# Kernel optimization log

Hardware: AMD Instinct MI355X
Metric: run time of the kernel (lower is better)

## Reference

```python
import jax, jax.numpy as jnp
import numpy as np

HIDDEN = 1024
BETA = 1.0
SPARSITY_THRESHOLD = 1.0


def _sparsemax(x):
    # Faithful port of the module's custom sparsemax (including its
    # nonstandard per-position tau). Operates over the last axis.
    n = x.shape[-1]
    z = x - jnp.max(x, axis=-1, keepdims=True)
    sum_z = jnp.sum(z, axis=-1, keepdims=True)
    step = (sum_z - 1.0) / n                       # step_size
    sorted_z = -jnp.sort(-z, axis=-1)              # descending sort
    cumsum_z = jnp.cumsum(sorted_z, axis=-1)
    is_gt = sorted_z > step
    rng = jnp.arange(1, n + 1, dtype=jnp.int32)
    k = jnp.max(rng * is_gt, axis=-1, keepdims=True).astype(x.dtype)
    tau = (cumsum_z - 1.0 - step * k) / k          # [.., n] per-position tau
    return jnp.clip(z - tau, 0.0)


def setup_inputs() -> dict:
    key = jax.random.key(0)
    kx, kq, kk, kv = jax.random.split(key, 4)
    B, S, D = 4, 2048, 1024
    x = jax.random.normal(kx, (B, S, D), dtype=jnp.float32)
    # torch Linear weight layout: [out_features, in_features]
    scale = 1.0 / np.sqrt(D)
    Wq = jax.random.normal(kq, (HIDDEN, D), dtype=jnp.float32) * scale
    Wk = jax.random.normal(kk, (HIDDEN, D), dtype=jnp.float32) * scale
    Wv = jax.random.normal(kv, (HIDDEN, D), dtype=jnp.float32) * scale
    return {"x": x, "Wq": Wq, "Wk": Wk, "Wv": Wv}


def reference(x, Wq, Wk, Wv):
    Q = jnp.einsum('bsd,hd->bsh', x, Wq)
    K = jnp.einsum('bsd,hd->bsh', x, Wk)
    V = jnp.einsum('bsd,hd->bsh', x, Wv)
    energy = jnp.einsum('bsh,bth->bst', Q, K) / jnp.sqrt(jnp.asarray(HIDDEN, x.dtype))
    scores = energy * BETA
    sparsity = jnp.mean(jnp.abs(x))
    attention = jax.lax.cond(
        sparsity < SPARSITY_THRESHOLD,
        _sparsemax,
        lambda s: jax.nn.softmax(s, axis=-1),
        scores,
    )
    return jnp.einsum('bst,bth->bsh', attention, V)
```

## Files before the change

### kernel.cpp

```cpp
#include <hip/hip_runtime.h>
#include <math.h>

#define B_   4
#define S_   2048
#define D_   1024
#define H_   1024
#define NROW 2048
#define TOTX 8388608.0f

typedef _Float16 f16x8 __attribute__((ext_vector_type(8)));
typedef float f32x4 __attribute__((ext_vector_type(4)));

__device__ __forceinline__ unsigned short f2h(float f) {
  _Float16 h = (_Float16)f;
  return __builtin_bit_cast(unsigned short, h);
}

#define GLD16(gp, lp)                                                            \
  __builtin_amdgcn_global_load_lds(                                              \
      (__attribute__((address_space(1))) void*)(gp),                             \
      (__attribute__((address_space(3))) void*)(lp), 16, 0, 0)

__global__ __launch_bounds__(256) void f2h_abs_kernel(const float* __restrict__ in,
                                                      unsigned short* __restrict__ out,
                                                      float* absOut, int n4) {
  int i0 = blockIdx.x * 256 + threadIdx.x;
  int stride = gridDim.x * 256;
  float s = 0.f;
  for (int i = i0; i < n4; i += stride) {
    float4 v = ((const float4*)in)[i];
    ushort4 o;
    o.x = f2h(v.x); o.y = f2h(v.y); o.z = f2h(v.z); o.w = f2h(v.w);
    ((ushort4*)out)[i] = o;
    s += fabsf(v.x) + fabsf(v.y) + fabsf(v.z) + fabsf(v.w);
  }
#pragma unroll
  for (int off = 32; off; off >>= 1) s += __shfl_xor(s, off);
  __shared__ float red[4];
  if ((threadIdx.x & 63) == 0) red[threadIdx.x >> 6] = s;
  __syncthreads();
  if (threadIdx.x == 0) atomicAdd(absOut, red[0] + red[1] + red[2] + red[3]);
}

__global__ __launch_bounds__(256) void f2h3_kernel(const float* __restrict__ a,
                                                   const float* __restrict__ b,
                                                   const float* __restrict__ c,
                                                   unsigned short* __restrict__ oa,
                                                   unsigned short* __restrict__ ob,
                                                   unsigned short* __restrict__ oc,
                                                   int n4) {
  int i = blockIdx.x * 256 + threadIdx.x;
  if (i >= n4) return;
  const float* in = (blockIdx.y == 0) ? a : (blockIdx.y == 1) ? b : c;
  unsigned short* out = (blockIdx.y == 0) ? oa : (blockIdx.y == 1) ? ob : oc;
  float4 v = ((const float4*)in)[i];
  ushort4 o;
  o.x = f2h(v.x); o.y = f2h(v.y); o.z = f2h(v.z); o.w = f2h(v.w);
  ((ushort4*)out)[i] = o;
}

__global__ __launch_bounds__(256) void transpose_h16(const unsigned short* __restrict__ in,
                                                     unsigned short* __restrict__ out,
                                                     int R, int C) {
  __shared__ unsigned short t[32][33];
  const int z = blockIdx.z;
  in  += (long long)z * R * C;
  out += (long long)z * R * C;
  const int c0 = blockIdx.x * 32, r0 = blockIdx.y * 32;
#pragma unroll
  for (int i = 0; i < 4; ++i) {
    int r = threadIdx.y + i * 8;
    t[r][threadIdx.x] = in[(long long)(r0 + r) * C + c0 + threadIdx.x];
  }
  __syncthreads();
#pragma unroll
  for (int i = 0; i < 4; ++i) {
    int r = threadIdx.y + i * 8;
    out[(long long)(c0 + r) * R + r0 + threadIdx.x] = t[threadIdx.x][r];
  }
}

template <int MI, bool OUT_F16>
__global__ __launch_bounds__(512, 2) void gemm8_nt(const unsigned short* __restrict__ A,
                                                   const unsigned short* __restrict__ B,
                                                   void* __restrict__ Cv,
                                                   int M, int N, int K,
                                                   long long sA, long long sB, long long sC,
                                                   float scale) {
  constexpr int BM  = MI * 32;
  constexpr int ASZ = BM * 32;
  constexpr int BSZ = 256 * 32;
  constexpr int TSZ = ASZ + BSZ;
  constexpr int MH  = MI / 2;

  const int bz = blockIdx.z;
  A += (long long)bz * sA;
  B += (long long)bz * sB;

  __shared__ __align__(16) unsigned short lds[2 * TSZ];

  const int tid = threadIdx.x;
  const int lane = tid & 63;
  const int w = tid >> 6;
  const int wr = w >> 2;
  const int wc = w & 3;
  const int m0 = blockIdx.y * BM, n0 = blockIdx.x * 256;

  f32x4 acc[MI][4] = {};

  const int srow = tid >> 2;
  const int scol = ((lane & 3) ^ ((lane >> 3) & 3)) * 8;
  const unsigned short* gA0 = A + (long long)(m0 + srow) * K + scol;
  const unsigned short* gA1 = gA0 + (long long)128 * K;
  const unsigned short* gB0 = B + (long long)(n0 + srow) * K + scol;
  const unsigned short* gB1 = gB0 + (long long)128 * K;
  const int wb = w * 512;

  const int fm = lane & 15;
  const int col8 = ((lane >> 4) ^ ((lane >> 1) & 3)) * 8;
  int aoff[MI], boff[4];
#pragma unroll
  for (int mi = 0; mi < MI; ++mi) aoff[mi] = (wr * (MI * 16) + mi * 16 + fm) * 32 + col8;
#pragma unroll
  for (int ni = 0; ni < 4; ++ni) boff[ni] = ASZ + (wc * 64 + ni * 16 + fm) * 32 + col8;

  const int nt = K >> 5;

#define STAGE(nb, k0)                                    \
  do {                                                   \
    unsigned short* L_ = lds + (nb) * TSZ;               \
    GLD16(gA0 + (k0), L_ + wb);                          \
    if (MI == 8) GLD16(gA1 + (k0), L_ + 4096 + wb);      \
    GLD16(gB0 + (k0), L_ + ASZ + wb);                    \
    GLD16(gB1 + (k0), L_ + ASZ + 4096 + wb);             \
  } while (0)

  STAGE(0, 0);
  STAGE(1, 32);
  if (MI == 8) asm volatile("s_waitcnt vmcnt(4)" ::: "memory");
  else         asm volatile("s_waitcnt vmcnt(3)" ::: "memory");
  __builtin_amdgcn_s_barrier();

  for (int t = 0; t < nt; ++t) {
    const unsigned short* L = lds + (t & 1) * TSZ;
    f16x8 af[MH], bf[4];
#pragma unroll
    for (int mi = 0; mi < MH; ++mi) af[mi] = *(const f16x8*)(L + aoff[mi]);
#pragma unroll
    for (int ni = 0; ni < 4; ++ni) bf[ni] = *(const f16x8*)(L + boff[ni]);
    __builtin_amdgcn_s_setprio(1);
#pragma unroll
    for (int mi = 0; mi < MH; ++mi)
#pragma unroll
      for (int ni = 0; ni < 4; ++ni)
        acc[mi][ni] = __builtin_amdgcn_mfma_f32_16x16x32_f16(af[mi], bf[ni],
                                                             acc[mi][ni], 0, 0, 0);
    __builtin_amdgcn_s_setprio(0);
    f16x8 ag[MH];
#pragma unroll
    for (int mi = 0; mi < MH; ++mi) ag[mi] = *(const f16x8*)(L + aoff[MH + mi]);
    asm volatile("s_waitcnt lgkmcnt(0)" ::: "memory");
    __builtin_amdgcn_sched_barrier(0);
    __builtin_amdgcn_s_barrier();
    if (t + 2 < nt) STAGE(t & 1, (t + 2) << 5);
    __builtin_amdgcn_s_setprio(1);
#pragma unroll
    for (int mi = 0; mi < MH; ++mi)
#pragma unroll
      for (int ni = 0; ni < 4; ++ni)
        acc[MH + mi][ni] = __builtin_amdgcn_mfma_f32_16x16x32_f16(ag[mi], bf[ni],
                                                                  acc[MH + mi][ni], 0, 0, 0);
    __builtin_amdgcn_s_setprio(0);
    if (t + 2 < nt) {
      if (MI == 8) asm volatile("s_waitcnt vmcnt(4)" ::: "memory");
      else         asm volatile("s_waitcnt vmcnt(3)" ::: "memory");
    } else if (t + 1 < nt) {
      asm volatile("s_waitcnt vmcnt(0)" ::: "memory");
    }
    __builtin_amdgcn_s_barrier();
  }
#undef STAGE

  const int cm = (lane >> 4) * 4;
  const int cn = lane & 15;
#pragma unroll
  for (int mi = 0; mi < MI; ++mi)
#pragma unroll
    for (int ni = 0; ni < 4; ++ni) {
#pragma unroll
      for (int r = 0; r < 4; ++r) {
        long long m = m0 + wr * (MI * 16) + mi * 16 + cm + r;
        long long n = n0 + wc * 64 + ni * 16 + cn;
        float v = acc[mi][ni][r] * scale;
        if (OUT_F16)
          ((unsigned short*)Cv)[(long long)bz * sC + m * N + n] = f2h(v);
        else
          ((float*)Cv)[(long long)bz * sC + m * N + n] = v;
      }
    }
}

template <int K, int J>
__device__ __forceinline__ void intra_s(float (&r)[32]) {
#pragma unroll
  for (int v = 0; v < 32; ++v)
    if ((v & J) == 0) {
      const int u = v | J;
      const bool dsc = ((v & K) == 0);
      float a = r[v], b = r[u];
      float mx = fmaxf(a, b), mn = fminf(a, b);
      r[v] = dsc ? mx : mn;
      r[u] = dsc ? mn : mx;
    }
}

template <int J>
__device__ __forceinline__ void intra_desc(float (&r)[32]) {
#pragma unroll
  for (int v = 0; v < 32; ++v)
    if ((v & J) == 0) {
      const int u = v | J;
      float a = r[v], b = r[u];
      r[v] = fmaxf(a, b);
      r[u] = fminf(a, b);
    }
}

template <int JL>
__device__ __forceinline__ void cross_desc(float (&r)[32], int lane, int bp32) {
  const bool keepmax = ((lane & JL) == 0);
  float b[32];
#pragma unroll
  for (int v = 0; v < 32; ++v) {
    int av = __builtin_bit_cast(int, r[v]);
    int bv;
    if constexpr (JL == 32)
      bv = __builtin_amdgcn_ds_bpermute(bp32, av);
    else
      bv = __builtin_amdgcn_ds_swizzle(av, (JL << 10) | 0x1F);
    b[v] = __builtin_bit_cast(float, bv);
  }
  __builtin_amdgcn_sched_barrier(0);
#pragma unroll
  for (int v = 0; v < 32; ++v) {
    float mx = fmaxf(r[v], b[v]), mn = fminf(r[v], b[v]);
    r[v] = keepmax ? mx : mn;
  }
}

__device__ __forceinline__ void signfix(float (&r)[32], unsigned fix) {
#pragma unroll
  for (int v = 0; v < 32; ++v)
    r[v] = __builtin_bit_cast(float, __builtin_bit_cast(unsigned, r[v]) ^ fix);
}

__global__ __launch_bounds__(256, 4) void attn_row_wave(const float* __restrict__ scores,
                                                        unsigned short* __restrict__ attn,
                                                        const float* __restrict__ absSum) {
  const int tid = threadIdx.x;
  const int lane = tid & 63;
  const int row = blockIdx.x * 4 + (tid >> 6);
  const float* rowp = scores + (long long)row * NROW;
  unsigned short* aout = attn + (long long)row * NROW;
  const int bp32 = (lane ^ 32) << 2;

  const float4* rp4 = (const float4*)rowp + lane * 8;
  float r[32];
  float lm = -INFINITY, lsraw = 0.f;
#pragma unroll
  for (int q = 0; q < 8; ++q) {
    float4 v = rp4[q];
    r[q * 4 + 0] = v.x; r[q * 4 + 1] = v.y;
    r[q * 4 + 2] = v.z; r[q * 4 + 3] = v.w;
    lm = fmaxf(lm, fmaxf(fmaxf(v.x, v.y), fmaxf(v.z, v.w)));
    lsraw += v.x + v.y + v.z + v.w;
  }
#pragma unroll
  for (int off = 32; off; off >>= 1) {
    lm = fmaxf(lm, __shfl_xor(lm, off, 64));
    lsraw += __shfl_xor(lsraw, off, 64);
  }

  const bool use_softmax = (absSum[0] * (1.0f / TOTX)) >= 1.0f;

  if (use_softmax) {
    float ls = 0.f;
#pragma unroll
    for (int v = 0; v < 32; ++v) { r[v] = expf(r[v] - lm); ls += r[v]; }
#pragma unroll
    for (int off = 32; off; off >>= 1) ls += __shfl_xor(ls, off, 64);
    float inv = 1.0f / ls;
    ushort4* op = (ushort4*)(aout + lane * 32);
#pragma unroll
    for (int q = 0; q < 8; ++q) {
      ushort4 o;
      o.x = f2h(r[q * 4 + 0] * inv); o.y = f2h(r[q * 4 + 1] * inv);
      o.z = f2h(r[q * 4 + 2] * inv); o.w = f2h(r[q * 4 + 3] * inv);
      op[q] = o;
    }
    return;
  }

#pragma unroll
  for (int v = 0; v < 32; ++v) r[v] -= lm;
  const float step = ((lsraw - (float)NROW * lm) - 1.0f) * (1.0f / (float)NROW);

  intra_s<2, 1>(r);
  intra_s<4, 2>(r); intra_s<4, 1>(r);
  intra_s<8, 4>(r); intra_s<8, 2>(r); intra_s<8, 1>(r);
  intra_s<16, 8>(r); intra_s<16, 4>(r); intra_s<16, 2>(r); intra_s<16, 1>(r);

  unsigned cur = (unsigned)(lane & 1) << 31;
  signfix(r, cur);
  intra_desc<16>(r); intra_desc<8>(r); intra_desc<4>(r);
  intra_desc<2>(r); intra_desc<1>(r);

  { unsigned want = (unsigned)(lane & 2) << 30;
    signfix(r, cur ^ want); cur = want; }
  cross_desc<1>(r, lane, bp32);
  intra_desc<16>(r); intra_desc<8>(r); intra_desc<4>(r);
  intra_desc<2>(r); intra_desc<1>(r);

  { unsigned want = (unsigned)(lane & 4) << 29;
    signfix(r, cur ^ want); cur = want; }
  cross_desc<2>(r, lane, bp32); cross_desc<1>(r, lane, bp32);
  intra_desc<16>(r); intra_desc<8>(r); intra_desc<4>(r);
  intra_desc<2>(r); intra_desc<1>(r);

  { unsigned want = (unsigned)(lane & 8) << 28;
    signfix(r, cur ^ want); cur = want; }
  cross_desc<4>(r, lane, bp32); cross_desc<2>(r, lane, bp32);
  cross_desc<1>(r, lane, bp32);
  intra_desc<16>(r); intra_desc<8>(r); intra_desc<4>(r);
  intra_desc<2>(r); intra_desc<1>(r);

  { unsigned want = (unsigned)(lane & 16) << 27;
    signfix(r, cur ^ want); cur = want; }
  cross_desc<8>(r, lane, bp32); cross_desc<4>(r, lane, bp32);
  cross_desc<2>(r, lane, bp32); cross_desc<1>(r, lane, bp32);
  intra_desc<16>(r); intra_desc<8>(r); intra_desc<4>(r);
  intra_desc<2>(r); intra_desc<1>(r);

  { unsigned want = (unsigned)(lane & 32) << 26;
    signfix(r, cur ^ want); cur = want; }
  cross_desc<16>(r, lane, bp32); cross_desc<8>(r, lane, bp32);
  cross_desc<4>(r, lane, bp32); cross_desc<2>(r, lane, bp32);
  cross_desc<1>(r, lane, bp32);
  intra_desc<16>(r); intra_desc<8>(r); intra_desc<4>(r);
  intra_desc<2>(r); intra_desc<1>(r);

  signfix(r, cur);
  cross_desc<32>(r, lane, bp32); cross_desc<16>(r, lane, bp32);
  cross_desc<8>(r, lane, bp32); cross_desc<4>(r, lane, bp32);
  cross_desc<2>(r, lane, bp32); cross_desc<1>(r, lane, bp32);
  intra_desc<16>(r); intra_desc<8>(r); intra_desc<4>(r);
  intra_desc<2>(r); intra_desc<1>(r);

  float lcnt = 0.f;
#pragma unroll
  for (int v = 0; v < 32; ++v) lcnt += (r[v] > step) ? 1.0f : 0.0f;
#pragma unroll
  for (int off = 32; off; off >>= 1) lcnt += __shfl_xor(lcnt, off, 64);
  const float kf = lcnt;

  float run = 0.f;
#pragma unroll
  for (int v = 0; v < 32; ++v) { run += r[v]; r[v] = run; }
  float pre = run;
#pragma unroll
  for (int off = 1; off < 64; off <<= 1) {
    float t = __shfl_up(pre, off, 64);
    if (lane >= off) pre += t;
  }
  pre -= run;
#pragma unroll
  for (int v = 0; v < 32; ++v) r[v] += pre;

  const float inv_k = 1.0f / kf;
  const float c1 = 1.0f + step * kf;

  unsigned long long up = (unsigned long long)rowp;
  asm volatile("" : "+v"(up));
  const float4* rp4e = (const float4*)up + lane * 8;
  ushort4* op = (ushort4*)(aout + lane * 32);
#pragma unroll
  for (int q = 0; q < 8; ++q) {
    float4 v = rp4e[q];
    ushort4 o;
    o.x = f2h(fmaxf((v.x - lm) - (r[q * 4 + 0] - c1) * inv_k, 0.0f));
    o.y = f2h(fmaxf((v.y - lm) - (r[q * 4 + 1] - c1) * inv_k, 0.0f));
    o.z = f2h(fmaxf((v.z - lm) - (r[q * 4 + 2] - c1) * inv_k, 0.0f));
    o.w = f2h(fmaxf((v.w - lm) - (r[q * 4 + 3] - c1) * inv_k, 0.0f));
    op[q] = o;
  }
}

extern "C" void kernel_launch(void* const* d_in, const int* in_sizes, int n_in,
                              void* d_out, int out_size, void* d_ws, size_t ws_size,
                              hipStream_t stream) {
  const float* x  = (const float*)d_in[0];
  const float* Wq = (const float*)d_in[1];
  const float* Wk = (const float*)d_in[2];
  const float* Wv = (const float*)d_in[3];
  float* out = (float*)d_out;

  const long long NX = (long long)B_ * S_ * D_;
  const long long NW = (long long)H_ * D_;

  char* base = (char*)d_ws;
  unsigned short* x16  = (unsigned short*)(base);
  unsigned short* Wq16 = (unsigned short*)(base + (16ll << 20));
  unsigned short* Wk16 = (unsigned short*)(base + (18ll << 20));
  unsigned short* Wv16 = (unsigned short*)(base + (20ll << 20));
  float*          Sc   = (float*)(base);
  unsigned short* Vt16 = (unsigned short*)(base + (64ll << 20));
  unsigned short* Q16  = (unsigned short*)(base + (80ll << 20));
  unsigned short* K16  = (unsigned short*)(base + (96ll << 20));
  unsigned short* V16  = (unsigned short*)(base + (112ll << 20));
  unsigned short* A16  = (unsigned short*)(base + (80ll << 20));
  float*          flag = (float*)(base + (144ll << 20));

  hipMemsetAsync(flag, 0, sizeof(float), stream);

  f2h_abs_kernel<<<1024, 256, 0, stream>>>(x, x16, flag, (int)(NX / 4));
  f2h3_kernel<<<dim3((int)(NW / 4 + 255) / 256, 3), 256, 0, stream>>>(
      Wq, Wk, Wv, Wq16, Wk16, Wv16, (int)(NW / 4));

  {
    dim3 grid(H_ / 256, (B_ * S_) / 128, 3);
    gemm8_nt<4, true><<<grid, 512, 0, stream>>>(x16, Wq16, Q16, B_ * S_, H_, D_,
                                                0, (long long)NW, (long long)(8ll << 20),
                                                1.0f);
  }

  {
    dim3 grid(H_ / 32, S_ / 32, B_);
    transpose_h16<<<grid, dim3(32, 8), 0, stream>>>(V16, Vt16, S_, H_);
  }

  {
    dim3 grid(S_ / 256, S_ / 256, B_);
    gemm8_nt<8, false><<<grid, 512, 0, stream>>>(Q16, K16, Sc, S_, S_, H_,
                                                 (long long)S_ * H_, (long long)S_ * H_,
                                                 (long long)S_ * S_, 1.0f / 32.0f);
  }

  attn_row_wave<<<(B_ * S_) / 4, 256, 0, stream>>>(Sc, A16, flag);

  {
    dim3 grid(H_ / 256, S_ / 128, B_);
    gemm8_nt<4, false><<<grid, 512, 0, stream>>>(A16, Vt16, out, S_, H_, S_,
                                                 (long long)S_ * S_, (long long)H_ * S_,
                                                 (long long)S_ * H_, 1.0f);
  }
}
```

Baseline: 338.0 us.

## Triple-buffer GEMM LDS pipeline and process two rows per wave in sparsemax

```diff
diff --git a/kernel.cpp b/kernel.cpp
--- a/kernel.cpp
+++ b/kernel.cpp
@@ -81,12 +81,13 @@
 }
 
 template <int MI, bool OUT_F16>
-__global__ __launch_bounds__(512, 2) void gemm8_nt(const unsigned short* __restrict__ A,
-                                                   const unsigned short* __restrict__ B,
-                                                   void* __restrict__ Cv,
-                                                   int M, int N, int K,
-                                                   long long sA, long long sB, long long sC,
-                                                   float scale) {
+__global__ __launch_bounds__(512, MI == 4 ? 4 : 2)
+void gemm8_nt(const unsigned short* __restrict__ A,
+              const unsigned short* __restrict__ B,
+              void* __restrict__ Cv,
+              int M, int N, int K,
+              long long sA, long long sB, long long sC,
+              float scale) {
   constexpr int BM  = MI * 32;
   constexpr int ASZ = BM * 32;
   constexpr int BSZ = 256 * 32;
@@ -97,7 +98,7 @@
   A += (long long)bz * sA;
   B += (long long)bz * sB;
 
-  __shared__ __align__(16) unsigned short lds[2 * TSZ];
+  __shared__ __align__(16) unsigned short lds[3 * TSZ];
 
   const int tid = threadIdx.x;
   const int lane = tid & 63;
@@ -126,28 +127,47 @@
 
   const int nt = K >> 5;
 
-#define STAGE(nb, k0)                                    \
-  do {                                                   \
-    unsigned short* L_ = lds + (nb) * TSZ;               \
-    GLD16(gA0 + (k0), L_ + wb);                          \
-    if (MI == 8) GLD16(gA1 + (k0), L_ + 4096 + wb);      \
-    GLD16(gB0 + (k0), L_ + ASZ + wb);                    \
-    GLD16(gB1 + (k0), L_ + ASZ + 4096 + wb);             \
+#define STAGE_ALL(nb, k0)                                      \
+  do {                                                         \
+    unsigned short* L_ = lds + (nb) * TSZ;                     \
+    if (MI == 8) {                                             \
+      GLD16(gA0 + (k0), L_ + wb);                              \
+      GLD16(gA1 + (k0), L_ + 4096 + wb);                       \
+      GLD16(gB0 + (k0), L_ + ASZ + wb);                        \
+      GLD16(gB1 + (k0), L_ + ASZ + 4096 + wb);                 \
+    } else {                                                   \
+      GLD16(gA0 + (k0), L_ + wb);                              \
+      GLD16(gB0 + (k0), L_ + ASZ + wb);                        \
+      GLD16(gB1 + (k0), L_ + ASZ + 4096 + wb);                 \
+    }                                                          \
   } while (0)
 
-  STAGE(0, 0);
-  STAGE(1, 32);
+  STAGE_ALL(0, 0);
+  STAGE_ALL(1, 32);
   if (MI == 8) asm volatile("s_waitcnt vmcnt(4)" ::: "memory");
   else         asm volatile("s_waitcnt vmcnt(3)" ::: "memory");
   __builtin_amdgcn_s_barrier();
 
+  int b0 = 0, b1 = 1, b2 = 2;
   for (int t = 0; t < nt; ++t) {
-    const unsigned short* L = lds + (t & 1) * TSZ;
+    const unsigned short* L = lds + b0 * TSZ;
+    unsigned short* Ls = lds + b2 * TSZ;
+    const bool st = (t + 2 < nt);
+    const int k2 = (t + 2) << 5;
+
     f16x8 af[MH], bf[4];
 #pragma unroll
     for (int mi = 0; mi < MH; ++mi) af[mi] = *(const f16x8*)(L + aoff[mi]);
 #pragma unroll
     for (int ni = 0; ni < 4; ++ni) bf[ni] = *(const f16x8*)(L + boff[ni]);
+    if (st) {
+      if (MI == 8) { GLD16(gA0 + k2, Ls + wb); GLD16(gA1 + k2, Ls + 4096 + wb); }
+      else         { GLD16(gA0 + k2, Ls + wb); GLD16(gB0 + k2, Ls + ASZ + wb); }
+    }
+    __builtin_amdgcn_sched_barrier(0);
+    __builtin_amdgcn_s_barrier();
+    asm volatile("s_waitcnt lgkmcnt(0)" ::: "memory");
+    __builtin_amdgcn_sched_barrier(0);
     __builtin_amdgcn_s_setprio(1);
 #pragma unroll
     for (int mi = 0; mi < MH; ++mi)
@@ -156,13 +176,25 @@
         acc[mi][ni] = __builtin_amdgcn_mfma_f32_16x16x32_f16(af[mi], bf[ni],
                                                              acc[mi][ni], 0, 0, 0);
     __builtin_amdgcn_s_setprio(0);
+    __builtin_amdgcn_s_barrier();
+
     f16x8 ag[MH];
 #pragma unroll
     for (int mi = 0; mi < MH; ++mi) ag[mi] = *(const f16x8*)(L + aoff[MH + mi]);
+    if (st) {
+      if (MI == 8) { GLD16(gB0 + k2, Ls + ASZ + wb); GLD16(gB1 + k2, Ls + ASZ + 4096 + wb); }
+      else         { GLD16(gB1 + k2, Ls + ASZ + 4096 + wb); }
+    }
+    if (st) {
+      if (MI == 8) asm volatile("s_waitcnt vmcnt(4)" ::: "memory");
+      else         asm volatile("s_waitcnt vmcnt(3)" ::: "memory");
+    } else if (t + 1 < nt) {
+      asm volatile("s_waitcnt vmcnt(0)" ::: "memory");
+    }
+    __builtin_amdgcn_sched_barrier(0);
+    __builtin_amdgcn_s_barrier();
     asm volatile("s_waitcnt lgkmcnt(0)" ::: "memory");
     __builtin_amdgcn_sched_barrier(0);
-    __builtin_amdgcn_s_barrier();
-    if (t + 2 < nt) STAGE(t & 1, (t + 2) << 5);
     __builtin_amdgcn_s_setprio(1);
 #pragma unroll
     for (int mi = 0; mi < MH; ++mi)
@@ -171,15 +203,11 @@
         acc[MH + mi][ni] = __builtin_amdgcn_mfma_f32_16x16x32_f16(ag[mi], bf[ni],
                                                                   acc[MH + mi][ni], 0, 0, 0);
     __builtin_amdgcn_s_setprio(0);
-    if (t + 2 < nt) {
-      if (MI == 8) asm volatile("s_waitcnt vmcnt(4)" ::: "memory");
-      else         asm volatile("s_waitcnt vmcnt(3)" ::: "memory");
-    } else if (t + 1 < nt) {
-      asm volatile("s_waitcnt vmcnt(0)" ::: "memory");
-    }
     __builtin_amdgcn_s_barrier();
-  }
-#undef STAGE
+
+    int tb = b0; b0 = b1; b1 = b2; b2 = tb;
+  }
+#undef STAGE_ALL
 
   const int cm = (lane >> 4) * 4;
   const int cn = lane & 15;
@@ -201,197 +229,234 @@
 }
 
 template <int K, int J>
-__device__ __forceinline__ void intra_s(float (&r)[32]) {
-#pragma unroll
-  for (int v = 0; v < 32; ++v)
-    if ((v & J) == 0) {
-      const int u = v | J;
-      const bool dsc = ((v & K) == 0);
-      float a = r[v], b = r[u];
-      float mx = fmaxf(a, b), mn = fminf(a, b);
-      r[v] = dsc ? mx : mn;
-      r[u] = dsc ? mn : mx;
-    }
+__device__ __forceinline__ void intra_s2(float (&r)[2][32]) {
+#pragma unroll
+  for (int h = 0; h < 2; ++h)
+#pragma unroll
+    for (int v = 0; v < 32; ++v)
+      if ((v & J) == 0) {
+        const int u = v | J;
+        const bool dsc = ((v & K) == 0);
+        float a = r[h][v], b = r[h][u];
+        float mx = fmaxf(a, b), mn = fminf(a, b);
+        r[h][v] = dsc ? mx : mn;
+        r[h][u] = dsc ? mn : mx;
+      }
 }
 
 template <int J>
-__device__ __forceinline__ void intra_desc(float (&r)[32]) {
-#pragma unroll
-  for (int v = 0; v < 32; ++v)
-    if ((v & J) == 0) {
-      const int u = v | J;
-      float a = r[v], b = r[u];
-      r[v] = fmaxf(a, b);
-      r[u] = fminf(a, b);
-    }
+__device__ __forceinline__ void intra_desc2(float (&r)[2][32]) {
+#pragma unroll
+  for (int h = 0; h < 2; ++h)
+#pragma unroll
+    for (int v = 0; v < 32; ++v)
+      if ((v & J) == 0) {
+        const int u = v | J;
+        float a = r[h][v], b = r[h][u];
+        r[h][v] = fmaxf(a, b);
+        r[h][u] = fminf(a, b);
+      }
 }
 
 template <int JL>
-__device__ __forceinline__ void cross_desc(float (&r)[32], int lane, int bp32) {
+__device__ __forceinline__ void cross_desc2(float (&r)[2][32], int lane, int bp32) {
   const bool keepmax = ((lane & JL) == 0);
-  float b[32];
-#pragma unroll
-  for (int v = 0; v < 32; ++v) {
-    int av = __builtin_bit_cast(int, r[v]);
-    int bv;
-    if constexpr (JL == 32)
-      bv = __builtin_amdgcn_ds_bpermute(bp32, av);
-    else
-      bv = __builtin_amdgcn_ds_swizzle(av, (JL << 10) | 0x1F);
-    b[v] = __builtin_bit_cast(float, bv);
-  }
+  float b[2][32];
+#pragma unroll
+  for (int h = 0; h < 2; ++h)
+#pragma unroll
+    for (int v = 0; v < 32; ++v) {
+      int av = __builtin_bit_cast(int, r[h][v]);
+      int bv;
+      if constexpr (JL == 32)
+        bv = __builtin_amdgcn_ds_bpermute(bp32, av);
+      else
+        bv = __builtin_amdgcn_ds_swizzle(av, (JL << 10) | 0x1F);
+      b[h][v] = __builtin_bit_cast(float, bv);
+    }
   __builtin_amdgcn_sched_barrier(0);
 #pragma unroll
-  for (int v = 0; v < 32; ++v) {
-    float mx = fmaxf(r[v], b[v]), mn = fminf(r[v], b[v]);
-    r[v] = keepmax ? mx : mn;
-  }
-}
-
-__device__ __forceinline__ void signfix(float (&r)[32], unsigned fix) {
-#pragma unroll
-  for (int v = 0; v < 32; ++v)
-    r[v] = __builtin_bit_cast(float, __builtin_bit_cast(unsigned, r[v]) ^ fix);
-}
-
-__global__ __launch_bounds__(256, 4) void attn_row_wave(const float* __restrict__ scores,
+  for (int h = 0; h < 2; ++h)
+#pragma unroll
+    for (int v = 0; v < 32; ++v) {
+      float mx = fmaxf(r[h][v], b[h][v]), mn = fminf(r[h][v], b[h][v]);
+      r[h][v] = keepmax ? mx : mn;
+    }
+}
+
+__device__ __forceinline__ void signfix2(float (&r)[2][32], unsigned fix) {
+#pragma unroll
+  for (int h = 0; h < 2; ++h)
+#pragma unroll
+    for (int v = 0; v < 32; ++v)
+      r[h][v] = __builtin_bit_cast(float, __builtin_bit_cast(unsigned, r[h][v]) ^ fix);
+}
+
+__global__ __launch_bounds__(256, 3) void attn_row_wave(const float* __restrict__ scores,
                                                         unsigned short* __restrict__ attn,
                                                         const float* __restrict__ absSum) {
   const int tid = threadIdx.x;
   const int lane = tid & 63;
-  const int row = blockIdx.x * 4 + (tid >> 6);
-  const float* rowp = scores + (long long)row * NROW;
-  unsigned short* aout = attn + (long long)row * NROW;
+  const int rbase = blockIdx.x * 8 + (tid >> 6) * 2;
+  const float* rowp = scores + (long long)rbase * NROW;
+  unsigned short* aout = attn + (long long)rbase * NROW;
   const int bp32 = (lane ^ 32) << 2;
 
-  const float4* rp4 = (const float4*)rowp + lane * 8;
-  float r[32];
-  float lm = -INFINITY, lsraw = 0.f;
-#pragma unroll
-  for (int q = 0; q < 8; ++q) {
-    float4 v = rp4[q];
-    r[q * 4 + 0] = v.x; r[q * 4 + 1] = v.y;
-    r[q * 4 + 2] = v.z; r[q * 4 + 3] = v.w;
-    lm = fmaxf(lm, fmaxf(fmaxf(v.x, v.y), fmaxf(v.z, v.w)));
-    lsraw += v.x + v.y + v.z + v.w;
+  float r[2][32];
+  float lm[2] = {-INFINITY, -INFINITY};
+  float ls[2] = {0.f, 0.f};
+#pragma unroll
+  for (int h = 0; h < 2; ++h) {
+    const float4* rp4 = (const float4*)(rowp + h * NROW) + lane * 8;
+#pragma unroll
+    for (int q = 0; q < 8; ++q) {
+      float4 v = rp4[q];
+      r[h][q * 4 + 0] = v.x; r[h][q * 4 + 1] = v.y;
+      r[h][q * 4 + 2] = v.z; r[h][q * 4 + 3] = v.w;
+      lm[h] = fmaxf(lm[h], fmaxf(fmaxf(v.x, v.y), fmaxf(v.z, v.w)));
+      ls[h] += v.x + v.y + v.z + v.w;
+    }
   }
 #pragma unroll
   for (int off = 32; off; off >>= 1) {
-    lm = fmaxf(lm, __shfl_xor(lm, off, 64));
-    lsraw += __shfl_xor(lsraw, off, 64);
+#pragma unroll
+    for (int h = 0; h < 2; ++h) {
+      lm[h] = fmaxf(lm[h], __shfl_xor(lm[h], off, 64));
+      ls[h] += __shfl_xor(ls[h], off, 64);
+    }
   }
 
   const bool use_softmax = (absSum[0] * (1.0f / TOTX)) >= 1.0f;
 
   if (use_softmax) {
-    float ls = 0.f;
-#pragma unroll
-    for (int v = 0; v < 32; ++v) { r[v] = expf(r[v] - lm); ls += r[v]; }
-#pragma unroll
-    for (int off = 32; off; off >>= 1) ls += __shfl_xor(ls, off, 64);
-    float inv = 1.0f / ls;
-    ushort4* op = (ushort4*)(aout + lane * 32);
-#pragma unroll
-    for (int q = 0; q < 8; ++q) {
-      ushort4 o;
-      o.x = f2h(r[q * 4 + 0] * inv); o.y = f2h(r[q * 4 + 1] * inv);
-      o.z = f2h(r[q * 4 + 2] * inv); o.w = f2h(r[q * 4 + 3] * inv);
-      op[q] = o;
+    float sum[2] = {0.f, 0.f};
+#pragma unroll
+    for (int h = 0; h < 2; ++h)
+#pragma unroll
+      for (int v = 0; v < 32; ++v) { r[h][v] = expf(r[h][v] - lm[h]); sum[h] += r[h][v]; }
+#pragma unroll
+    for (int off = 32; off; off >>= 1)
+#pragma unroll
+      for (int h = 0; h < 2; ++h) sum[h] += __shfl_xor(sum[h], off, 64);
+#pragma unroll
+    for (int h = 0; h < 2; ++h) {
+      float inv = 1.0f / sum[h];
+      ushort4* op = (ushort4*)(aout + h * NROW + lane * 32);
+#pragma unroll
+      for (int q = 0; q < 8; ++q) {
+        ushort4 o;
+        o.x = f2h(r[h][q * 4 + 0] * inv); o.y = f2h(r[h][q * 4 + 1] * inv);
+        o.z = f2h(r[h][q * 4 + 2] * inv); o.w = f2h(r[h][q * 4 + 3] * inv);
+        op[q] = o;
+      }
     }
     return;
   }
 
-#pragma unroll
-  for (int v = 0; v < 32; ++v) r[v] -= lm;
-  const float step = ((lsraw - (float)NROW * lm) - 1.0f) * (1.0f / (float)NROW);
-
-  intra_s<2, 1>(r);
-  intra_s<4, 2>(r); intra_s<4, 1>(r);
-  intra_s<8, 4>(r); intra_s<8, 2>(r); intra_s<8, 1>(r);
-  intra_s<16, 8>(r); intra_s<16, 4>(r); intra_s<16, 2>(r); intra_s<16, 1>(r);
+  float step[2];
+#pragma unroll
+  for (int h = 0; h < 2; ++h) {
+#pragma unroll
+    for (int v = 0; v < 32; ++v) r[h][v] -= lm[h];
+    step[h] = ((ls[h] - (float)NROW * lm[h]) - 1.0f) * (1.0f / (float)NROW);
+  }
+
+  intra_s2<2, 1>(r);
+  intra_s2<4, 2>(r); intra_s2<4, 1>(r);
+  intra_s2<8, 4>(r); intra_s2<8, 2>(r); intra_s2<8, 1>(r);
+  intra_s2<16, 8>(r); intra_s2<16, 4>(r); intra_s2<16, 2>(r); intra_s2<16, 1>(r);
 
   unsigned cur = (unsigned)(lane & 1) << 31;
-  signfix(r, cur);
-  intra_desc<16>(r); intra_desc<8>(r); intra_desc<4>(r);
-  intra_desc<2>(r); intra_desc<1>(r);
+  signfix2(r, cur);
+  intra_desc2<16>(r); intra_desc2<8>(r); intra_desc2<4>(r);
+  intra_desc2<2>(r); intra_desc2<1>(r);
 
   { unsigned want = (unsigned)(lane & 2) << 30;
-    signfix(r, cur ^ want); cur = want; }
-  cross_desc<1>(r, lane, bp32);
-  intra_desc<16>(r); intra_desc<8>(r); intra_desc<4>(r);
-  intra_desc<2>(r); intra_desc<1>(r);
+    signfix2(r, cur ^ want); cur = want; }
+  cross_desc2<1>(r, lane, bp32);
+  intra_desc2<16>(r); intra_desc2<8>(r); intra_desc2<4>(r);
+  intra_desc2<2>(r); intra_desc2<1>(r);
 
   { unsigned want = (unsigned)(lane & 4) << 29;
-    signfix(r, cur ^ want); cur = want; }
-  cross_desc<2>(r, lane, bp32); cross_desc<1>(r, lane, bp32);
-  intra_desc<16>(r); intra_desc<8>(r); intra_desc<4>(r);
-  intra_desc<2>(r); intra_desc<1>(r);
+    signfix2(r, cur ^ want); cur = want; }
+  cross_desc2<2>(r, lane, bp32); cross_desc2<1>(r, lane, bp32);
+  intra_desc2<16>(r); intra_desc2<8>(r); intra_desc2<4>(r);
+  intra_desc2<2>(r); intra_desc2<1>(r);
 
   { unsigned want = (unsigned)(lane & 8) << 28;
-    signfix(r, cur ^ want); cur = want; }
-  cross_desc<4>(r, lane, bp32); cross_desc<2>(r, lane, bp32);
-  cross_desc<1>(r, lane, bp32);
-  intra_desc<16>(r); intra_desc<8>(r); intra_desc<4>(r);
-  intra_desc<2>(r); intra_desc<1>(r);
+    signfix2(r, cur ^ want); cur = want; }
+  cross_desc2<4>(r, lane, bp32); cross_desc2<2>(r, lane, bp32);
+  cross_desc2<1>(r, lane, bp32);
+  intra_desc2<16>(r); intra_desc2<8>(r); intra_desc2<4>(r);
+  intra_desc2<2>(r); intra_desc2<1>(r);
 
   { unsigned want = (unsigned)(lane & 16) << 27;
-    signfix(r, cur ^ want); cur = want; }
-  cross_desc<8>(r, lane, bp32); cross_desc<4>(r, lane, bp32);
-  cross_desc<2>(r, lane, bp32); cross_desc<1>(r, lane, bp32);
-  intra_desc<16>(r); intra_desc<8>(r); intra_desc<4>(r);
-  intra_desc<2>(r); intra_desc<1>(r);
+    signfix2(r, cur ^ want); cur = want; }
+  cross_desc2<8>(r, lane, bp32); cross_desc2<4>(r, lane, bp32);
+  cross_desc2<2>(r, lane, bp32); cross_desc2<1>(r, lane, bp32);
+  intra_desc2<16>(r); intra_desc2<8>(r); intra_desc2<4>(r);
+  intra_desc2<2>(r); intra_desc2<1>(r);
 
   { unsigned want = (unsigned)(lane & 32) << 26;
-    signfix(r, cur ^ want); cur = want; }
-  cross_desc<16>(r, lane, bp32); cross_desc<8>(r, lane, bp32);
-  cross_desc<4>(r, lane, bp32); cross_desc<2>(r, lane, bp32);
-  cross_desc<1>(r, lane, bp32);
-  intra_desc<16>(r); intra_desc<8>(r); intra_desc<4>(r);
-  intra_desc<2>(r); intra_desc<1>(r);
-
-  signfix(r, cur);
-  cross_desc<32>(r, lane, bp32); cross_desc<16>(r, lane, bp32);
-  cross_desc<8>(r, lane, bp32); cross_desc<4>(r, lane, bp32);
-  cross_desc<2>(r, lane, bp32); cross_desc<1>(r, lane, bp32);
-  intra_desc<16>(r); intra_desc<8>(r); intra_desc<4>(r);
-  intra_desc<2>(r); intra_desc<1>(r);
-
-  float lcnt = 0.f;
-#pragma unroll
-  for (int v = 0; v < 32; ++v) lcnt += (r[v] > step) ? 1.0f : 0.0f;
-#pragma unroll
-  for (int off = 32; off; off >>= 1) lcnt += __shfl_xor(lcnt, off, 64);
-  const float kf = lcnt;
-
-  float run = 0.f;
-#pragma unroll
-  for (int v = 0; v < 32; ++v) { run += r[v]; r[v] = run; }
-  float pre = run;
-#pragma unroll
-  for (int off = 1; off < 64; off <<= 1) {
-    float t = __shfl_up(pre, off, 64);
-    if (lane >= off) pre += t;
-  }
-  pre -= run;
-#pragma unroll
-  for (int v = 0; v < 32; ++v) r[v] += pre;
-
-  const float inv_k = 1.0f / kf;
-  const float c1 = 1.0f + step * kf;
+    signfix2(r, cur ^ want); cur = want; }
+  cross_desc2<16>(r, lane, bp32); cross_desc2<8>(r, lane, bp32);
+  cross_desc2<4>(r, lane, bp32); cross_desc2<2>(r, lane, bp32);
+  cross_desc2<1>(r, lane, bp32);
+  intra_desc2<16>(r); intra_desc2<8>(r); intra_desc2<4>(r);
+  intra_desc2<2>(r); intra_desc2<1>(r);
+
+  signfix2(r, cur);
+  cross_desc2<32>(r, lane, bp32); cross_desc2<16>(r, lane, bp32);
+  cross_desc2<8>(r, lane, bp32); cross_desc2<4>(r, lane, bp32);
+  cross_desc2<2>(r, lane, bp32); cross_desc2<1>(r, lane, bp32);
+  intra_desc2<16>(r); intra_desc2<8>(r); intra_desc2<4>(r);
+  intra_desc2<2>(r); intra_desc2<1>(r);
+
+  float kf[2];
+#pragma unroll
+  for (int h = 0; h < 2; ++h) {
+    float lcnt = 0.f;
+#pragma unroll
+    for (int v = 0; v < 32; ++v) lcnt += (r[h][v] > step[h]) ? 1.0f : 0.0f;
+#pragma unroll
+    for (int off = 32; off; off >>= 1) lcnt += __shfl_xor(lcnt, off, 64);
+    kf[h] = lcnt;
+  }
+
+#pragma unroll
+  for (int h = 0; h < 2; ++h) {
+    float run = 0.f;
+#pragma unroll
+    for (int v = 0; v < 32; ++v) { run += r[h][v]; r[h][v] = run; }
+    float pre = run;
+#pragma unroll
+    for (int off = 1; off < 64; off <<= 1) {
+      float t = __shfl_up(pre, off, 64);
+      if (lane >= off) pre += t;
+    }
+    pre -= run;
+#pragma unroll
+    for (int v = 0; v < 32; ++v) r[h][v] += pre;
+  }
 
   unsigned long long up = (unsigned long long)rowp;
   asm volatile("" : "+v"(up));
-  const float4* rp4e = (const float4*)up + lane * 8;
-  ushort4* op = (ushort4*)(aout + lane * 32);
-#pragma unroll
-  for (int q = 0; q < 8; ++q) {
-    float4 v = rp4e[q];
-    ushort4 o;
-    o.x = f2h(fmaxf((v.x - lm) - (r[q * 4 + 0] - c1) * inv_k, 0.0f));
-    o.y = f2h(fmaxf((v.y - lm) - (r[q * 4 + 1] - c1) * inv_k, 0.0f));
-    o.z = f2h(fmaxf((v.z - lm) - (r[q * 4 + 2] - c1) * inv_k, 0.0f));
-    o.w = f2h(fmaxf((v.w - lm) - (r[q * 4 + 3] - c1) * inv_k, 0.0f));
-    op[q] = o;
+#pragma unroll
+  for (int h = 0; h < 2; ++h) {
+    const float inv_k = 1.0f / kf[h];
+    const float c1 = 1.0f + step[h] * kf[h];
+    const float4* rp4e = (const float4*)(up + (unsigned long long)h * NROW * 4) + lane * 8;
+    ushort4* op = (ushort4*)(aout + h * NROW + lane * 32);
+#pragma unroll
+    for (int q = 0; q < 8; ++q) {
+      float4 v = rp4e[q];
+      ushort4 o;
+      o.x = f2h(fmaxf((v.x - lm[h]) - (r[h][q * 4 + 0] - c1) * inv_k, 0.0f));
+      o.y = f2h(fmaxf((v.y - lm[h]) - (r[h][q * 4 + 1] - c1) * inv_k, 0.0f));
+      o.z = f2h(fmaxf((v.z - lm[h]) - (r[h][q * 4 + 2] - c1) * inv_k, 0.0f));
+      o.w = f2h(fmaxf((v.w - lm[h]) - (r[h][q * 4 + 3] - c1) * inv_k, 0.0f));
+      op[q] = o;
+    }
   }
 }
 
@@ -445,7 +510,7 @@
                                                  (long long)S_ * S_, 1.0f / 32.0f);
   }
 
-  attn_row_wave<<<(B_ * S_) / 4, 256, 0, stream>>>(Sc, A16, flag);
+  attn_row_wave<<<(B_ * S_) / 8, 256, 0, stream>>>(Sc, A16, flag);
 
   {
     dim3 grid(H_ / 256, S_ / 128, B_);
```

New measurement: 365.3 us. 1.08x slower.

## Sort each sparsemax row with a full workgroup instead of one wave

Applied to the files above, without the earlier changes.

```diff
diff --git a/kernel.cpp b/kernel.cpp
--- a/kernel.cpp
+++ b/kernel.cpp
@@ -10,6 +10,7 @@
 
 typedef _Float16 f16x8 __attribute__((ext_vector_type(8)));
 typedef float f32x4 __attribute__((ext_vector_type(4)));
+typedef unsigned short us8 __attribute__((ext_vector_type(8)));
 
 __device__ __forceinline__ unsigned short f2h(float f) {
   _Float16 h = (_Float16)f;
@@ -201,9 +202,9 @@
 }
 
 template <int K, int J>
-__device__ __forceinline__ void intra_s(float (&r)[32]) {
-#pragma unroll
-  for (int v = 0; v < 32; ++v)
+__device__ __forceinline__ void p_intra_s(float (&r)[8]) {
+#pragma unroll
+  for (int v = 0; v < 8; ++v)
     if ((v & J) == 0) {
       const int u = v | J;
       const bool dsc = ((v & K) == 0);
@@ -215,9 +216,9 @@
 }
 
 template <int J>
-__device__ __forceinline__ void intra_desc(float (&r)[32]) {
-#pragma unroll
-  for (int v = 0; v < 32; ++v)
+__device__ __forceinline__ void p_intra_d(float (&r)[8]) {
+#pragma unroll
+  for (int v = 0; v < 8; ++v)
     if ((v & J) == 0) {
       const int u = v | J;
       float a = r[v], b = r[u];
@@ -226,173 +227,187 @@
     }
 }
 
-template <int JL>
-__device__ __forceinline__ void cross_desc(float (&r)[32], int lane, int bp32) {
-  const bool keepmax = ((lane & JL) == 0);
-  float b[32];
-#pragma unroll
-  for (int v = 0; v < 32; ++v) {
+template <int LJ>
+__device__ __forceinline__ void p_cross_d(float (&r)[8], int lane, int bp32) {
+  const bool keepmax = ((lane & LJ) == 0);
+  float b[8];
+#pragma unroll
+  for (int v = 0; v < 8; ++v) {
     int av = __builtin_bit_cast(int, r[v]);
     int bv;
-    if constexpr (JL == 32)
+    if constexpr (LJ == 32)
       bv = __builtin_amdgcn_ds_bpermute(bp32, av);
     else
-      bv = __builtin_amdgcn_ds_swizzle(av, (JL << 10) | 0x1F);
+      bv = __builtin_amdgcn_ds_swizzle(av, (LJ << 10) | 0x1F);
     b[v] = __builtin_bit_cast(float, bv);
   }
   __builtin_amdgcn_sched_barrier(0);
 #pragma unroll
-  for (int v = 0; v < 32; ++v) {
+  for (int v = 0; v < 8; ++v) {
     float mx = fmaxf(r[v], b[v]), mn = fminf(r[v], b[v]);
     r[v] = keepmax ? mx : mn;
   }
 }
 
-__device__ __forceinline__ void signfix(float (&r)[32], unsigned fix) {
-#pragma unroll
-  for (int v = 0; v < 32; ++v)
+__device__ __forceinline__ void p_lds_d(float (&r)[8], float* LB, int tid, int wv, int WJ) {
+  const bool keepmax = ((wv & WJ) == 0);
+  __syncthreads();
+  float4* my = (float4*)(LB + tid * 8);
+  my[0] = make_float4(r[0], r[1], r[2], r[3]);
+  my[1] = make_float4(r[4], r[5], r[6], r[7]);
+  __syncthreads();
+  const float4* pp = (const float4*)(LB + (tid ^ (WJ << 6)) * 8);
+  float4 p0 = pp[0], p1 = pp[1];
+  float p[8] = {p0.x, p0.y, p0.z, p0.w, p1.x, p1.y, p1.z, p1.w};
+#pragma unroll
+  for (int v = 0; v < 8; ++v) {
+    float mx = fmaxf(r[v], p[v]), mn = fminf(r[v], p[v]);
+    r[v] = keepmax ? mx : mn;
+  }
+}
+
+__device__ __forceinline__ void sf8(float (&r)[8], unsigned fix) {
+#pragma unroll
+  for (int v = 0; v < 8; ++v)
     r[v] = __builtin_bit_cast(float, __builtin_bit_cast(unsigned, r[v]) ^ fix);
 }
 
-__global__ __launch_bounds__(256, 4) void attn_row_wave(const float* __restrict__ scores,
+__global__ __launch_bounds__(256, 6) void attn_row_wave(const float* __restrict__ scores,
                                                         unsigned short* __restrict__ attn,
                                                         const float* __restrict__ absSum) {
+  __shared__ float LB[2048];
+  __shared__ float red[8];
   const int tid = threadIdx.x;
   const int lane = tid & 63;
-  const int row = blockIdx.x * 4 + (tid >> 6);
+  const int wv = tid >> 6;
+  const int row = blockIdx.x;
   const float* rowp = scores + (long long)row * NROW;
   unsigned short* aout = attn + (long long)row * NROW;
   const int bp32 = (lane ^ 32) << 2;
 
-  const float4* rp4 = (const float4*)rowp + lane * 8;
-  float r[32];
-  float lm = -INFINITY, lsraw = 0.f;
-#pragma unroll
-  for (int q = 0; q < 8; ++q) {
-    float4 v = rp4[q];
-    r[q * 4 + 0] = v.x; r[q * 4 + 1] = v.y;
-    r[q * 4 + 2] = v.z; r[q * 4 + 3] = v.w;
-    lm = fmaxf(lm, fmaxf(fmaxf(v.x, v.y), fmaxf(v.z, v.w)));
-    lsraw += v.x + v.y + v.z + v.w;
-  }
+  const float4* rp4 = (const float4*)rowp + tid * 2;
+  float4 v0 = rp4[0], v1 = rp4[1];
+  float r[8] = {v0.x, v0.y, v0.z, v0.w, v1.x, v1.y, v1.z, v1.w};
+
+  float lm = fmaxf(fmaxf(fmaxf(r[0], r[1]), fmaxf(r[2], r[3])),
+                   fmaxf(fmaxf(r[4], r[5]), fmaxf(r[6], r[7])));
+  float ls = r[0] + r[1] + r[2] + r[3] + r[4] + r[5] + r[6] + r[7];
 #pragma unroll
   for (int off = 32; off; off >>= 1) {
     lm = fmaxf(lm, __shfl_xor(lm, off, 64));
-    lsraw += __shfl_xor(lsraw, off, 64);
-  }
+    ls += __shfl_xor(ls, off, 64);
+  }
+  if (lane == 0) { red[wv] = lm; red[4 + wv] = ls; }
+  __syncthreads();
+  lm = fmaxf(fmaxf(red[0], red[1]), fmaxf(red[2], red[3]));
+  ls = red[4] + red[5] + red[6] + red[7];
 
   const bool use_softmax = (absSum[0] * (1.0f / TOTX)) >= 1.0f;
 
   if (use_softmax) {
-    float ls = 0.f;
-#pragma unroll
-    for (int v = 0; v < 32; ++v) { r[v] = expf(r[v] - lm); ls += r[v]; }
-#pragma unroll
-    for (int off = 32; off; off >>= 1) ls += __shfl_xor(ls, off, 64);
-    float inv = 1.0f / ls;
-    ushort4* op = (ushort4*)(aout + lane * 32);
-#pragma unroll
-    for (int q = 0; q < 8; ++q) {
-      ushort4 o;
-      o.x = f2h(r[q * 4 + 0] * inv); o.y = f2h(r[q * 4 + 1] * inv);
-      o.z = f2h(r[q * 4 + 2] * inv); o.w = f2h(r[q * 4 + 3] * inv);
-      op[q] = o;
-    }
+    float s = 0.f;
+#pragma unroll
+    for (int v = 0; v < 8; ++v) { r[v] = expf(r[v] - lm); s += r[v]; }
+#pragma unroll
+    for (int off = 32; off; off >>= 1) s += __shfl_xor(s, off, 64);
+    __syncthreads();
+    if (lane == 0) red[wv] = s;
+    __syncthreads();
+    float inv = 1.0f / (red[0] + red[1] + red[2] + red[3]);
+    us8 o;
+#pragma unroll
+    for (int v = 0; v < 8; ++v) o[v] = f2h(r[v] * inv);
+    *(us8*)(aout + tid * 8) = o;
     return;
   }
 
 #pragma unroll
-  for (int v = 0; v < 32; ++v) r[v] -= lm;
-  const float step = ((lsraw - (float)NROW * lm) - 1.0f) * (1.0f / (float)NROW);
-
-  intra_s<2, 1>(r);
-  intra_s<4, 2>(r); intra_s<4, 1>(r);
-  intra_s<8, 4>(r); intra_s<8, 2>(r); intra_s<8, 1>(r);
-  intra_s<16, 8>(r); intra_s<16, 4>(r); intra_s<16, 2>(r); intra_s<16, 1>(r);
-
-  unsigned cur = (unsigned)(lane & 1) << 31;
-  signfix(r, cur);
-  intra_desc<16>(r); intra_desc<8>(r); intra_desc<4>(r);
-  intra_desc<2>(r); intra_desc<1>(r);
-
-  { unsigned want = (unsigned)(lane & 2) << 30;
-    signfix(r, cur ^ want); cur = want; }
-  cross_desc<1>(r, lane, bp32);
-  intra_desc<16>(r); intra_desc<8>(r); intra_desc<4>(r);
-  intra_desc<2>(r); intra_desc<1>(r);
-
-  { unsigned want = (unsigned)(lane & 4) << 29;
-    signfix(r, cur ^ want); cur = want; }
-  cross_desc<2>(r, lane, bp32); cross_desc<1>(r, lane, bp32);
-  intra_desc<16>(r); intra_desc<8>(r); intra_desc<4>(r);
-  intra_desc<2>(r); intra_desc<1>(r);
-
-  { unsigned want = (unsigned)(lane & 8) << 28;
-    signfix(r, cur ^ want); cur = want; }
-  cross_desc<4>(r, lane, bp32); cross_desc<2>(r, lane, bp32);
-  cross_desc<1>(r, lane, bp32);
-  intra_desc<16>(r); intra_desc<8>(r); intra_desc<4>(r);
-  intra_desc<2>(r); intra_desc<1>(r);
-
-  { unsigned want = (unsigned)(lane & 16) << 27;
-    signfix(r, cur ^ want); cur = want; }
-  cross_desc<8>(r, lane, bp32); cross_desc<4>(r, lane, bp32);
-  cross_desc<2>(r, lane, bp32); cross_desc<1>(r, lane, bp32);
-  intra_desc<16>(r); intra_desc<8>(r); intra_desc<4>(r);
-  intra_desc<2>(r); intra_desc<1>(r);
-
-  { unsigned want = (unsigned)(lane & 32) << 26;
-    signfix(r, cur ^ want); cur = want; }
-  cross_desc<16>(r, lane, bp32); cross_desc<8>(r, lane, bp32);
-  cross_desc<4>(r, lane, bp32); cross_desc<2>(r, lane, bp32);
-  cross_desc<1>(r, lane, bp32);
-  intra_desc<16>(r); intra_desc<8>(r); intra_desc<4>(r);
-  intra_desc<2>(r); intra_desc<1>(r);
-
-  signfix(r, cur);
-  cross_desc<32>(r, lane, bp32); cross_desc<16>(r, lane, bp32);
-  cross_desc<8>(r, lane, bp32); cross_desc<4>(r, lane, bp32);
-  cross_desc<2>(r, lane, bp32); cross_desc<1>(r, lane, bp32);
-  intra_desc<16>(r); intra_desc<8>(r); intra_desc<4>(r);
-  intra_desc<2>(r); intra_desc<1>(r);
+  for (int v = 0; v < 8; ++v) r[v] -= lm;
+  const float step = ((ls - (float)NROW * lm) - 1.0f) * (1.0f / (float)NROW);
+
+  p_intra_s<2, 1>(r);
+  p_intra_s<4, 2>(r); p_intra_s<4, 1>(r);
+
+  unsigned cur;
+  cur = (tid & 1) ? 0x80000000u : 0u; sf8(r, cur);
+  p_intra_d<4>(r); p_intra_d<2>(r); p_intra_d<1>(r);
+  { unsigned want = (tid & 2) ? 0x80000000u : 0u; sf8(r, cur ^ want); cur = want; }
+  p_cross_d<1>(r, lane, bp32);
+  p_intra_d<4>(r); p_intra_d<2>(r); p_intra_d<1>(r);
+  { unsigned want = (tid & 4) ? 0x80000000u : 0u; sf8(r, cur ^ want); cur = want; }
+  p_cross_d<2>(r, lane, bp32); p_cross_d<1>(r, lane, bp32);
+  p_intra_d<4>(r); p_intra_d<2>(r); p_intra_d<1>(r);
+  { unsigned want = (tid & 8) ? 0x80000000u : 0u; sf8(r, cur ^ want); cur = want; }
+  p_cross_d<4>(r, lane, bp32); p_cross_d<2>(r, lane, bp32); p_cross_d<1>(r, lane, bp32);
+  p_intra_d<4>(r); p_intra_d<2>(r); p_intra_d<1>(r);
+  { unsigned want = (tid & 16) ? 0x80000000u : 0u; sf8(r, cur ^ want); cur = want; }
+  p_cross_d<8>(r, lane, bp32); p_cross_d<4>(r, lane, bp32);
+  p_cross_d<2>(r, lane, bp32); p_cross_d<1>(r, lane, bp32);
+  p_intra_d<4>(r); p_intra_d<2>(r); p_intra_d<1>(r);
+  { unsigned want = (tid & 32) ? 0x80000000u : 0u; sf8(r, cur ^ want); cur = want; }
+  p_cross_d<16>(r, lane, bp32); p_cross_d<8>(r, lane, bp32); p_cross_d<4>(r, lane, bp32);
+  p_cross_d<2>(r, lane, bp32); p_cross_d<1>(r, lane, bp32);
+  p_intra_d<4>(r); p_intra_d<2>(r); p_intra_d<1>(r);
+  { unsigned want = (tid & 64) ? 0x80000000u : 0u; sf8(r, cur ^ want); cur = want; }
+  p_cross_d<32>(r, lane, bp32); p_cross_d<16>(r, lane, bp32); p_cross_d<8>(r, lane, bp32);
+  p_cross_d<4>(r, lane, bp32); p_cross_d<2>(r, lane, bp32); p_cross_d<1>(r, lane, bp32);
+  p_intra_d<4>(r); p_intra_d<2>(r); p_intra_d<1>(r);
+  { unsigned want = (tid & 128) ? 0x80000000u : 0u; sf8(r, cur ^ want); cur = want; }
+  p_lds_d(r, LB, tid, wv, 1);
+  p_cross_d<32>(r, lane, bp32); p_cross_d<16>(r, lane, bp32); p_cross_d<8>(r, lane, bp32);
+  p_cross_d<4>(r, lane, bp32); p_cross_d<2>(r, lane, bp32); p_cross_d<1>(r, lane, bp32);
+  p_intra_d<4>(r); p_intra_d<2>(r); p_intra_d<1>(r);
+  sf8(r, cur); cur = 0;
+  p_lds_d(r, LB, tid, wv, 2);
+  p_lds_d(r, LB, tid, wv, 1);
+  p_cross_d<32>(r, lane, bp32); p_cross_d<16>(r, lane, bp32); p_cross_d<8>(r, lane, bp32);
+  p_cross_d<4>(r, lane, bp32); p_cross_d<2>(r, lane, bp32); p_cross_d<1>(r, lane, bp32);
+  p_intra_d<4>(r); p_intra_d<2>(r); p_intra_d<1>(r);
 
   float lcnt = 0.f;
 #pragma unroll
-  for (int v = 0; v < 32; ++v) lcnt += (r[v] > step) ? 1.0f : 0.0f;
+  for (int v = 0; v < 8; ++v) lcnt += (r[v] > step) ? 1.0f : 0.0f;
 #pragma unroll
   for (int off = 32; off; off >>= 1) lcnt += __shfl_xor(lcnt, off, 64);
-  const float kf = lcnt;
 
   float run = 0.f;
 #pragma unroll
-  for (int v = 0; v < 32; ++v) { run += r[v]; r[v] = run; }
-  float pre = run;
+  for (int v = 0; v < 8; ++v) { run += r[v]; r[v] = run; }
+  float sc = run;
 #pragma unroll
   for (int off = 1; off < 64; off <<= 1) {
-    float t = __shfl_up(pre, off, 64);
-    if (lane >= off) pre += t;
-  }
-  pre -= run;
-#pragma unroll
-  for (int v = 0; v < 32; ++v) r[v] += pre;
-
-  const float inv_k = 1.0f / kf;
-  const float c1 = 1.0f + step * kf;
+    float t = __shfl_up(sc, off, 64);
+    if (lane >= off) sc += t;
+  }
+  const float tex = sc - run;
+
+  __syncthreads();
+  if (lane == 0)  red[wv] = lcnt;
+  if (lane == 63) red[4 + wv] = sc;
+  __syncthreads();
+  const float kf = red[0];
+  const float kfull = red[0] + red[1] + red[2] + red[3];
+  (void)kf;
+  float wex = 0.f;
+  if (wv > 0) wex += red[4];
+  if (wv > 1) wex += red[5];
+  if (wv > 2) wex += red[6];
+#pragma unroll
+  for (int v = 0; v < 8; ++v) r[v] += tex + wex;
+
+  const float inv_k = 1.0f / kfull;
+  const float c1 = 1.0f + step * kfull;
 
   unsigned long long up = (unsigned long long)rowp;
   asm volatile("" : "+v"(up));
-  const float4* rp4e = (const float4*)up + lane * 8;
-  ushort4* op = (ushort4*)(aout + lane * 32);
-#pragma unroll
-  for (int q = 0; q < 8; ++q) {
-    float4 v = rp4e[q];
-    ushort4 o;
-    o.x = f2h(fmaxf((v.x - lm) - (r[q * 4 + 0] - c1) * inv_k, 0.0f));
-    o.y = f2h(fmaxf((v.y - lm) - (r[q * 4 + 1] - c1) * inv_k, 0.0f));
-    o.z = f2h(fmaxf((v.z - lm) - (r[q * 4 + 2] - c1) * inv_k, 0.0f));
-    o.w = f2h(fmaxf((v.w - lm) - (r[q * 4 + 3] - c1) * inv_k, 0.0f));
-    op[q] = o;
-  }
+  const float4* rp4e = (const float4*)up + tid * 2;
+  float4 w0 = rp4e[0], w1 = rp4e[1];
+  float zo[8] = {w0.x, w0.y, w0.z, w0.w, w1.x, w1.y, w1.z, w1.w};
+  us8 o;
+#pragma unroll
+  for (int v = 0; v < 8; ++v)
+    o[v] = f2h(fmaxf((zo[v] - lm) - (r[v] - c1) * inv_k, 0.0f));
+  *(us8*)(aout + tid * 8) = o;
 }
 
 extern "C" void kernel_launch(void* const* d_in, const int* in_sizes, int n_in,
@@ -445,7 +460,7 @@
                                                  (long long)S_ * S_, 1.0f / 32.0f);
   }
 
-  attn_row_wave<<<(B_ * S_) / 4, 256, 0, stream>>>(Sc, A16, flag);
+  attn_row_wave<<<B_ * S_, 256, 0, stream>>>(Sc, A16, flag);
 
   {
     dim3 grid(H_ / 256, S_ / 128, B_);
```

Measured after the change: 354.2 us. +4.8%, slower.

## Fuse V transpose into projection GEMM epilogue and shrink QK^T tile

Applied to the files above, without the earlier changes.

```diff
diff --git a/kernel.cpp b/kernel.cpp
--- a/kernel.cpp
+++ b/kernel.cpp
@@ -59,31 +59,11 @@
   ((ushort4*)out)[i] = o;
 }
 
-__global__ __launch_bounds__(256) void transpose_h16(const unsigned short* __restrict__ in,
-                                                     unsigned short* __restrict__ out,
-                                                     int R, int C) {
-  __shared__ unsigned short t[32][33];
-  const int z = blockIdx.z;
-  in  += (long long)z * R * C;
-  out += (long long)z * R * C;
-  const int c0 = blockIdx.x * 32, r0 = blockIdx.y * 32;
-#pragma unroll
-  for (int i = 0; i < 4; ++i) {
-    int r = threadIdx.y + i * 8;
-    t[r][threadIdx.x] = in[(long long)(r0 + r) * C + c0 + threadIdx.x];
-  }
-  __syncthreads();
-#pragma unroll
-  for (int i = 0; i < 4; ++i) {
-    int r = threadIdx.y + i * 8;
-    out[(long long)(c0 + r) * R + r0 + threadIdx.x] = t[threadIdx.x][r];
-  }
-}
-
 template <int MI, bool OUT_F16>
 __global__ __launch_bounds__(512, 2) void gemm8_nt(const unsigned short* __restrict__ A,
                                                    const unsigned short* __restrict__ B,
                                                    void* __restrict__ Cv,
+                                                   unsigned short* __restrict__ VT,
                                                    int M, int N, int K,
                                                    long long sA, long long sB, long long sC,
                                                    float scale) {
@@ -183,6 +163,23 @@
 
   const int cm = (lane >> 4) * 4;
   const int cn = lane & 15;
+  if (VT != nullptr && bz == 2) {
+#pragma unroll
+    for (int mi = 0; mi < MI; ++mi)
+#pragma unroll
+      for (int ni = 0; ni < 4; ++ni) {
+        int m = m0 + wr * (MI * 16) + mi * 16 + cm;
+        int n = n0 + wc * 64 + ni * 16 + cn;
+        int b = m >> 11, s = m & 2047;
+        ushort4 o;
+        o.x = f2h(acc[mi][ni][0] * scale);
+        o.y = f2h(acc[mi][ni][1] * scale);
+        o.z = f2h(acc[mi][ni][2] * scale);
+        o.w = f2h(acc[mi][ni][3] * scale);
+        *(ushort4*)(VT + (long long)b * (H_ * S_) + (long long)n * S_ + s) = o;
+      }
+    return;
+  }
 #pragma unroll
   for (int mi = 0; mi < MI; ++mi)
 #pragma unroll
@@ -416,7 +413,6 @@
   unsigned short* Vt16 = (unsigned short*)(base + (64ll << 20));
   unsigned short* Q16  = (unsigned short*)(base + (80ll << 20));
   unsigned short* K16  = (unsigned short*)(base + (96ll << 20));
-  unsigned short* V16  = (unsigned short*)(base + (112ll << 20));
   unsigned short* A16  = (unsigned short*)(base + (80ll << 20));
   float*          flag = (float*)(base + (144ll << 20));
 
@@ -428,19 +424,16 @@
 
   {
     dim3 grid(H_ / 256, (B_ * S_) / 128, 3);
-    gemm8_nt<4, true><<<grid, 512, 0, stream>>>(x16, Wq16, Q16, B_ * S_, H_, D_,
+    gemm8_nt<4, true><<<grid, 512, 0, stream>>>(x16, Wq16, Q16, Vt16,
+                                                B_ * S_, H_, D_,
                                                 0, (long long)NW, (long long)(8ll << 20),
                                                 1.0f);
   }
 
   {
-    dim3 grid(H_ / 32, S_ / 32, B_);
-    transpose_h16<<<grid, dim3(32, 8), 0, stream>>>(V16, Vt16, S_, H_);
-  }
-
-  {
-    dim3 grid(S_ / 256, S_ / 256, B_);
-    gemm8_nt<8, false><<<grid, 512, 0, stream>>>(Q16, K16, Sc, S_, S_, H_,
+    dim3 grid(S_ / 256, S_ / 128, B_);
+    gemm8_nt<4, false><<<grid, 512, 0, stream>>>(Q16, K16, Sc, nullptr,
+                                                 S_, S_, H_,
                                                  (long long)S_ * H_, (long long)S_ * H_,
                                                  (long long)S_ * S_, 1.0f / 32.0f);
   }
@@ -449,7 +442,8 @@
 
   {
     dim3 grid(H_ / 256, S_ / 128, B_);
-    gemm8_nt<4, false><<<grid, 512, 0, stream>>>(A16, Vt16, out, S_, H_, S_,
+    gemm8_nt<4, false><<<grid, 512, 0, stream>>>(A16, Vt16, out, nullptr,
+                                                 S_, H_, S_,
                                                  (long long)S_ * S_, (long long)H_ * S_,
                                                  (long long)S_ * H_, 1.0f);
   }
```

New measurement: 335.8 us. Within noise of the previous version (-0.6%).
